# Kernel tuning notes

Measured on AMD Instinct MI355X. Metric: run time of the kernel, lower is better.

The kernel has to match this reference:

```python
import jax, jax.numpy as jnp
import numpy as np

K = 3  # kernel_size

def _extract_patches(x):
    # x: (b, n, h, w) -> (b, n, K*K, h, w), stride=1, padding=1 (zeros), row-major kernel order like nn.Unfold
    b, n, h, w = x.shape
    xp = jnp.pad(x, ((0, 0), (0, 0), (1, 1), (1, 1)))
    slices = [xp[:, :, i:i + h, j:j + w] for i in range(K) for j in range(K)]
    return jnp.stack(slices, axis=2)

def _conv3x3(x, w, b):
    # x: (b, cin, h, w), w: (cout, cin, 3, 3)
    y = jax.lax.conv_general_dilated(
        x, w, window_strides=(1, 1), padding=((1, 1), (1, 1)),
        dimension_numbers=('NCHW', 'OIHW', 'NCHW'))
    return y + b[None, :, None, None]

def setup_inputs() -> dict:
    key = jax.random.key(0)
    ks = jax.random.split(key, 6)
    b, n, h, w = 8, 256, 64, 64
    cout, r = 256, 4
    cm = n // r
    s = lambda fan: 1.0 / np.sqrt(fan)
    return {
        'x':    jax.random.normal(ks[0], (b, n, h, w), jnp.float32),
        'w_c1': jax.random.normal(ks[1], (cm, n), jnp.float32) * s(n),
        'b_c1': jnp.zeros((cm,), jnp.float32),
        'w_c2': jax.random.normal(ks[2], (n, cm), jnp.float32) * s(cm),
        'b_c2': jnp.zeros((n,), jnp.float32),
        'w_d1': jax.random.normal(ks[3], (cm, n, 3, 3), jnp.float32) * s(n * 9),
        'b_d1': jnp.zeros((cm,), jnp.float32),
        'w_d2': jax.random.normal(ks[4], (K * K, cm), jnp.float32) * s(cm),
        'b_d2': jnp.zeros((K * K,), jnp.float32),
        'W':    jax.random.normal(ks[5], (cout, n, K * K), jnp.float32) * s(n * K * K),
    }

def reference(x, w_c1, b_c1, w_c2, b_c2, w_d1, b_d1, w_d2, b_d2, W):
    # channel attention branch: 1x1 -> ReLU -> 1x1, output (b, n, h, w)
    yc = jax.nn.relu(jnp.einsum('bnhw,mn->bmhw', x, w_c1) + b_c1[None, :, None, None])
    c = jnp.einsum('bmhw,nm->bnhw', yc, w_c2) + b_c2[None, :, None, None]
    # kernel (spatial) attention branch: 3x3 -> ReLU -> 1x1, output (b, K*K, h, w)
    yd = jax.nn.relu(_conv3x3(x, w_d1, b_d1))
    d = jnp.einsum('bmhw,km->bkhw', yd, w_d2) + b_d2[None, :, None, None]
    # unfold and modulate: (b, n, K*K, h, w)
    patches = _extract_patches(x)
    attn = 1.0 + jnp.tanh(d[:, None, :, :, :] + c[:, :, None, :, :])
    # conv3d with (out, in, K*K, 1, 1) weight == per-pixel contraction over (n, K*K)
    out = jnp.einsum('bnkhw,onk->bohw', patches * attn, W)
    return out
```

## Files before the change

### kernel.cpp

```cpp
#include <hip/hip_runtime.h>
#include <hip/hip_bf16.h>
#include <stdint.h>

typedef __attribute__((ext_vector_type(8))) short bf16x8;
typedef __attribute__((ext_vector_type(4))) short bf16x4;
typedef __attribute__((ext_vector_type(4))) float f32x4;
typedef __attribute__((ext_vector_type(4))) int   i32x4;
typedef __attribute__((ext_vector_type(2))) int   i32x2;

#define DEV static __device__ __forceinline__

DEV float bf2f(short s) {
    unsigned u = ((unsigned)(unsigned short)s) << 16;
    return __builtin_bit_cast(float, u);
}
DEV short f2bf(float f) {
    unsigned u = __builtin_bit_cast(unsigned, f);
    unsigned r = u + 0x7fffu + ((u >> 16) & 1u);
    return (short)(r >> 16);
}
DEV unsigned cvt_pk_bf16(float lo, float hi) {
    unsigned r;
    asm("v_cvt_pk_bf16_f32 %0, %1, %2" : "=v"(r) : "v"(lo), "v"(hi));
    return r;
}

#define PTOT 32768
#define NEXP2 (-2.885390081777927f)

#define WS_WC1F 0
#define WS_WC2F 32768
#define WS_WD1F 65536
#define WS_WF   360448
#define WS_EKT  1540096
#define WS_EN   2719744
#define WS_XT   19496960

__global__ __launch_bounds__(256) void k_prep_all(const float* __restrict__ W, const float* __restrict__ w_d1,
                                              const float* __restrict__ w_c1, const float* __restrict__ w_c2,
                                              const float* __restrict__ x,
                                              short* __restrict__ Wf, short* __restrict__ wd1f,
                                              short* __restrict__ wc1f, short* __restrict__ wc2f,
                                              short* __restrict__ xT8) {
    __shared__ short t[64 * 74];
    const int tid = threadIdx.x;
    if (blockIdx.x < 3008) {
        int tt = blockIdx.x * 256 + tid;
        if (tt < 589824) {
            int i = tt & 7, lane = (tt >> 3) & 63, ot = (tt >> 9) & 15, kt = tt >> 13;
            int o = ot * 16 + (lane & 15);
            int n = (kt & 7) * 32 + (lane >> 4) * 8 + i;
            Wf[tt] = f2bf(2.0f * W[o * 2304 + n * 9 + (kt >> 3)]);
        } else if (tt < 589824 + 147456) {
            int t2 = tt - 589824;
            int i = t2 & 7, lane = (t2 >> 3) & 63, wv = (t2 >> 9) & 3, kc = t2 >> 11;
            int m = wv * 16 + (lane & 15);
            int n = (kc & 7) * 32 + (lane >> 4) * 8 + i;
            wd1f[t2] = f2bf(w_d1[m * 2304 + n * 9 + (kc >> 3)]);
        } else if (tt < 589824 + 147456 + 16384) {
            int t3 = tt - (589824 + 147456);
            int i = t3 & 7, lane = (t3 >> 3) & 63, wv = (t3 >> 9) & 3, s = t3 >> 11;
            int m = wv * 16 + (lane & 15);
            int n = s * 32 + (lane >> 4) * 8 + i;
            wc1f[t3] = f2bf(w_c1[m * 256 + n]);
        } else if (tt < 589824 + 147456 + 32768) {
            int t4 = tt - (589824 + 147456 + 16384);
            int i = t4 & 7, lane = (t4 >> 3) & 63, ot = (t4 >> 9) & 15, s = t4 >> 13;
            int o = ot * 16 + (lane & 15);
            int kk = s * 32 + (lane >> 4) * 8 + i;
            wc2f[t4] = f2bf(w_c2[o * 64 + kk]);
        }
        return;
    }
    const int bid = blockIdx.x - 3008;
    const int rw = ((bid & 7) << 6) + (bid >> 3);
    const int b = rw >> 6, hr = rw & 63;
    const int hp = hr + 1;
    #define XI(HP, NP, WP) ((((size_t)(b) * 66 + (HP)) * 32 + (NP)) * 66 + (WP)) * 8
    if (tid < 64) {
        int np = tid & 31, wp = (tid & 32) ? 65 : 0;
        *(i32x4*)(xT8 + XI(hp, np, wp)) = i32x4{0, 0, 0, 0};
    }
    if (hr == 0) {
        for (int i = tid; i < 2 * 32 * 66; i += 256) {
            int pl = (i >= 32 * 66) ? 65 : 0;
            int rem = (i >= 32 * 66) ? i - 32 * 66 : i;
            int np = rem / 66, wp = rem - np * 66;
            *(i32x4*)(xT8 + XI(pl, np, wp)) = i32x4{0, 0, 0, 0};
        }
    }
    const int dn = tid >> 6, w = tid & 63;
    for (int p = 0; p < 4; ++p) {
        __syncthreads();
        #pragma unroll
        for (int jj = 0; jj < 16; ++jj) {
            int n = p * 64 + dn * 16 + jj;
            t[w * 74 + dn * 16 + jj] = f2bf(x[(((size_t)(b * 256 + n) * 64) + hr) * 64 + w]);
        }
        __syncthreads();
        #pragma unroll
        for (int q = 0; q < 2; ++q) {
            int nl = q * 4 + dn;
            *(bf16x8*)(xT8 + XI(hp, p * 8 + nl, w + 1)) = *(const bf16x8*)(t + w * 74 + nl * 8);
        }
    }
    #undef XI
}

#define BR_YD_OFF  9216
#define BR_ENT_OFF (BR_YD_OFF + 17152)
#define BR_TOTAL   (BR_ENT_OFF + 33792)

__global__ __launch_bounds__(512, 4) void k_branch(const short* __restrict__ xT8,
        const float* __restrict__ b_c1, const float* __restrict__ b_c2,
        const float* __restrict__ b_d1, const float* __restrict__ w_d2, const float* __restrict__ b_d2,
        const short* __restrict__ wc1f, const short* __restrict__ wc2f, const short* __restrict__ wd1f,
        short* __restrict__ enF, float* __restrict__ ekT) {
    extern __shared__ char smem[];
    short* yc  = (short*)smem;
    float* ydl = (float*)(smem + BR_YD_OFF);
    short* ent = (short*)(smem + BR_ENT_OFF);

    const int rw = ((blockIdx.x & 7) << 6) + (blockIdx.x >> 3);
    const int b = rw >> 6, h = rw & 63;
    const int p0 = rw << 6;
    const int tid = threadIdx.x;
    const int lane = tid & 63, wave = tid >> 6;
    const int l16 = lane & 15, lg = lane >> 4;
    const int wn = wave & 3, wm = wave >> 2;
    const int cm = wn * 16 + l16;
    const size_t b66h = (size_t)(b * 66 + h);
    const int wcol = wm * 32 + l16;

    #define CONV_A(DST, KC) {                                                           \
        int k9_ = (KC) >> 3;                                                            \
        int kh_ = (k9_ * 11) >> 5, kw_ = k9_ - 3 * kh_;                                 \
        const short* xa_ = xT8 + (((b66h + kh_) * 32 + ((KC) & 7) * 4 + lg) * 66        \
                                  + wcol + kw_) * 8;                                    \
        DST[0] = *(const bf16x8*)(xa_);                                                 \
        DST[1] = *(const bf16x8*)(xa_ + 128);                                           \
    }

    {
        f32x4 acc[2] = {};
        const short* wp_ = wc1f + wn * 512 + lane * 8;
        const short* xg1 = xT8 + (((b66h + 1) * 32 + lg) * 66 + wcol + 1) * 8;
        bf16x8 bcur = *(const bf16x8*)(wp_);
        bf16x8 a0 = *(const bf16x8*)(xg1), a1 = *(const bf16x8*)(xg1 + 128);
        #pragma unroll
        for (int s = 0; s < 8; ++s) {
            bf16x8 bc = bcur, c0 = a0, c1 = a1;
            if (s < 7) {
                bcur = *(const bf16x8*)(wp_ + (s + 1) * 2048);
                a0 = *(const bf16x8*)(xg1 + (s + 1) * 2112);
                a1 = *(const bf16x8*)(xg1 + (s + 1) * 2112 + 128);
            }
            acc[0] = __builtin_amdgcn_mfma_f32_16x16x32_bf16(c0, bc, acc[0], 0, 0, 0);
            acc[1] = __builtin_amdgcn_mfma_f32_16x16x32_bf16(c1, bc, acc[1], 0, 0, 0);
        }
        float bias = b_c1[cm];
        #pragma unroll
        for (int mt = 0; mt < 2; ++mt)
            #pragma unroll
            for (int r = 0; r < 4; ++r) {
                int px = wm * 32 + mt * 16 + lg * 4 + r;
                float v = acc[mt][r] + bias;
                yc[px * 72 + cm] = f2bf(v > 0.f ? v : 0.f);
            }
    }

    {
        f32x4 acc[2] = {};
        const short* wp_ = wd1f + wn * 512 + lane * 8;
        bf16x8 b0 = *(const bf16x8*)(wp_);
        bf16x8 b1 = *(const bf16x8*)(wp_ + 2048);
        bf16x8 b2 = *(const bf16x8*)(wp_ + 4096);
        bf16x8 aA[2], aB[2], aC[2];
        CONV_A(aA, 0) CONV_A(aB, 1) CONV_A(aC, 2)
        for (int kc = 0; kc < 72; kc += 3) {
            {
                bf16x8 c0 = aA[0], c1 = aA[1], bc = b0;
                int cn = (kc + 3 < 72) ? kc + 3 : 71;
                CONV_A(aA, cn)
                b0 = *(const bf16x8*)(wp_ + cn * 2048);
                acc[0] = __builtin_amdgcn_mfma_f32_16x16x32_bf16(c0, bc, acc[0], 0, 0, 0);
                acc[1] = __builtin_amdgcn_mfma_f32_16x16x32_bf16(c1, bc, acc[1], 0, 0, 0);
            }
            {
                bf16x8 c0 = aB[0], c1 = aB[1], bc = b1;
                int cn = (kc + 4 < 72) ? kc + 4 : 71;
                CONV_A(aB, cn)
                b1 = *(const bf16x8*)(wp_ + cn * 2048);
                acc[0] = __builtin_amdgcn_mfma_f32_16x16x32_bf16(c0, bc, acc[0], 0, 0, 0);
                acc[1] = __builtin_amdgcn_mfma_f32_16x16x32_bf16(c1, bc, acc[1], 0, 0, 0);
            }
            {
                bf16x8 c0 = aC[0], c1 = aC[1], bc = b2;
                int cn = (kc + 5 < 72) ? kc + 5 : 71;
                CONV_A(aC, cn)
                b2 = *(const bf16x8*)(wp_ + cn * 2048);
                acc[0] = __builtin_amdgcn_mfma_f32_16x16x32_bf16(c0, bc, acc[0], 0, 0, 0);
                acc[1] = __builtin_amdgcn_mfma_f32_16x16x32_bf16(c1, bc, acc[1], 0, 0, 0);
            }
        }
        float bias = b_d1[cm];
        #pragma unroll
        for (int mt = 0; mt < 2; ++mt)
            #pragma unroll
            for (int r = 0; r < 4; ++r) {
                int px = wm * 32 + mt * 16 + lg * 4 + r;
                float v = acc[mt][r] + bias;
                ydl[px * 67 + cm] = v > 0.f ? v : 0.f;
            }
    }
    #undef CONV_A
    __syncthreads();

    {
        f32x4 acc[2][4] = {};
        #pragma unroll
        for (int s = 0; s < 2; ++s) {
            int k0 = s * 32;
            bf16x8 afr[2], bfr[4];
            #pragma unroll
            for (int mt = 0; mt < 2; ++mt)
                afr[mt] = *(const bf16x8*)(yc + (wm * 32 + mt * 16 + l16) * 72 + k0 + lg * 8);
            #pragma unroll
            for (int nt = 0; nt < 4; ++nt)
                bfr[nt] = *(const bf16x8*)(wc2f + s * 8192 + (wn * 4 + nt) * 512 + lane * 8);
            #pragma unroll
            for (int mt = 0; mt < 2; ++mt)
                #pragma unroll
                for (int nt = 0; nt < 4; ++nt)
                    acc[mt][nt] = __builtin_amdgcn_mfma_f32_16x16x32_bf16(afr[mt], bfr[nt], acc[mt][nt], 0, 0, 0);
        }
        #pragma unroll
        for (int nt = 0; nt < 4; ++nt) {
            int nc = wn * 64 + nt * 16 + l16;
            float bias = b_c2[nc];
            #pragma unroll
            for (int mt = 0; mt < 2; ++mt)
                #pragma unroll
                for (int r = 0; r < 4; ++r) {
                    int px = wm * 32 + mt * 16 + lg * 4 + r;
                    float cv = acc[mt][nt][r] + bias;
                    ent[px * 264 + nc] = f2bf(exp2f(NEXP2 * cv));
                }
        }
    }

    for (int t = tid; t < 576; t += 512) {
        int k = t >> 6, px = t & 63;
        float sum = b_d2[k];
        const float* yr = ydl + px * 67;
        const float* wr = w_d2 + k * 64;
        #pragma unroll 8
        for (int m = 0; m < 64; ++m) sum += yr[m] * wr[m];
        ekT[(size_t)k * PTOT + p0 + px] = exp2f(NEXP2 * sum);
    }
    __syncthreads();

    for (int i = tid; i < 2048; i += 512) {
        int px = i & 63, seg = i >> 6;
        *(bf16x8*)(enF + (size_t)p0 * 256 + (seg >> 2) * 2048 + (seg & 3) * 512 + px * 8)
            = *(const bf16x8*)(ent + px * 264 + seg * 8);
    }
}

#define FN5_Z1    4096
#define FN5_EKL   8192
#define FN5_TOTAL 10496

__global__ __launch_bounds__(512, 4) void k_final(const short* __restrict__ xT8,
        const short* __restrict__ Wf, const short* __restrict__ enF, const float* __restrict__ ekT,
        float* __restrict__ out) {
    extern __shared__ char smem[];
    short* z0  = (short*)smem;
    short* z1  = (short*)(smem + FN5_Z1);
    float* ekl = (float*)(smem + FN5_EKL);

    const int rw = ((blockIdx.x & 7) << 6) + (blockIdx.x >> 3);
    const int b = rw >> 6, h = rw & 63;
    const int p0 = rw << 6;
    const int tid = threadIdx.x;
    const int lane = tid & 63, wave = tid >> 6;
    const int l16 = lane & 15, lg = lane >> 4;

    for (int i = tid; i < 576; i += 512)
        ekl[i] = ekT[(size_t)(i >> 6) * PTOT + p0 + (i & 63)];

    const size_t b66h = (size_t)(b * 66 + h);
    const int zpx = lane;
    const int wh = wave >> 1, wl = wave & 1;
    const short* xb0 = xT8 + (b66h * 32 + wh) * 528 + zpx * 8 + wl * 4;
    bf16x4 e_regs[8];
    {
        const short* enb = enF + (size_t)p0 * 256 + wh * 512 + zpx * 8 + wl * 4;
        #pragma unroll
        for (int c8 = 0; c8 < 8; ++c8) e_regs[c8] = *(const bf16x4*)(enb + c8 * 2048);
    }
    const int zwoff = (zpx >> 4) * 512 + ((zpx & 15) + wh * 16) * 8 + wl * 4;
    const short* wb0 = Wf + (wave * 2 + 0) * 512 + lane * 8;
    const short* wb1 = Wf + (wave * 2 + 1) * 512 + lane * 8;

    bf16x4 xr;
    #define XLOAD(KC2) {                                                                \
        int k3_ = (KC2) >> 3, c8_ = (KC2) & 7;                                          \
        int kh_ = (k3_ * 11) >> 5, kw_ = k3_ - 3 * kh_;                                 \
        xr = *(const bf16x4*)(xb0 + kh_ * 16896 + c8_ * 2112 + kw_ * 8);                \
    }
    #define ZBUILD(ZBUF, EKROW, EIDX) {                                                 \
        bf16x4 er = e_regs[EIDX];                                                       \
        float ekv = ekl[(EKROW) * 64 + zpx];                                            \
        float q0 = __builtin_fmaf(ekv, bf2f(er[0]), 1.0f);                              \
        float q1 = __builtin_fmaf(ekv, bf2f(er[1]), 1.0f);                              \
        float q2 = __builtin_fmaf(ekv, bf2f(er[2]), 1.0f);                              \
        float q3 = __builtin_fmaf(ekv, bf2f(er[3]), 1.0f);                              \
        i32x2 zz;                                                                       \
        zz[0] = cvt_pk_bf16(bf2f(xr[0]) * __builtin_amdgcn_rcpf(q0),                    \
                            bf2f(xr[1]) * __builtin_amdgcn_rcpf(q1));                   \
        zz[1] = cvt_pk_bf16(bf2f(xr[2]) * __builtin_amdgcn_rcpf(q2),                    \
                            bf2f(xr[3]) * __builtin_amdgcn_rcpf(q3));                   \
        *(i32x2*)((ZBUF) + zwoff) = zz;                                                 \
    }

    bf16x8 Be[2], Bo[2];
    Be[0] = *(const bf16x8*)(wb0);          Be[1] = *(const bf16x8*)(wb1);
    Bo[0] = *(const bf16x8*)(wb0 + 8192);   Bo[1] = *(const bf16x8*)(wb1 + 8192);
    XLOAD(0)
    __syncthreads();
    ZBUILD(z0, 0, 0)
    XLOAD(1)
    __syncthreads();

    f32x4 acc[4][2] = {};

    #define STEP(C8, P1, P2, EKROW) {                                                   \
        short* zcur = ((C8) & 1) ? z1 : z0;                                             \
        short* znxt = ((C8) & 1) ? z0 : z1;                                             \
        bf16x8 bc0, bc1;                                                                \
        if ((C8) & 1) { bc0 = Bo[0]; bc1 = Bo[1]; } else { bc0 = Be[0]; bc1 = Be[1]; }  \
        if (P2) {    \
            int kb2_ = (k3 * 8 + (C8) + 2) * 8192;                                      \
            if ((C8) & 1) { Bo[0] = *(const bf16x8*)(wb0 + kb2_);                       \
                            Bo[1] = *(const bf16x8*)(wb1 + kb2_); }                     \
            else          { Be[0] = *(const bf16x8*)(wb0 + kb2_);                       \
                            Be[1] = *(const bf16x8*)(wb1 + kb2_); }                     \
        }                                                                               \
        if (P1) ZBUILD(znxt, EKROW, ((C8) + 1) & 7)                                     \
        if (P2) XLOAD(k3 * 8 + (C8) + 2)                                                \
        bf16x8 afr[4];                                                                  \
        _Pragma("unroll")                                                               \
        for (int mt = 0; mt < 4; ++mt)                                                  \
            afr[mt] = *(const bf16x8*)(zcur + mt * 512 + lane * 8);                     \
        __builtin_amdgcn_s_setprio(1);                                                  \
        _Pragma("unroll")                                                               \
        for (int mt = 0; mt < 4; ++mt) {                                                \
            acc[mt][0] = __builtin_amdgcn_mfma_f32_16x16x32_bf16(afr[mt], bc0, acc[mt][0], 0, 0, 0); \
            acc[mt][1] = __builtin_amdgcn_mfma_f32_16x16x32_bf16(afr[mt], bc1, acc[mt][1], 0, 0, 0); \
        }                                                                               \
        __builtin_amdgcn_s_setprio(0);                                                  \
        __syncthreads();                                                                \
    }

    for (int k3 = 0; k3 < 8; ++k3) {
        STEP(0, 1, 1, k3) STEP(1, 1, 1, k3) STEP(2, 1, 1, k3) STEP(3, 1, 1, k3)
        STEP(4, 1, 1, k3) STEP(5, 1, 1, k3) STEP(6, 1, 1, k3) STEP(7, 1, 1, k3 + 1)
    }
    {
        const int k3 = 8;
        STEP(0, 1, 1, k3) STEP(1, 1, 1, k3) STEP(2, 1, 1, k3) STEP(3, 1, 1, k3)
        STEP(4, 1, 1, k3) STEP(5, 1, 1, k3) STEP(6, 1, 0, k3) STEP(7, 0, 0, k3)
    }
    #undef STEP
    #undef ZBUILD
    #undef XLOAD

    #pragma unroll
    for (int mt = 0; mt < 4; ++mt)
        #pragma unroll
        for (int nt = 0; nt < 2; ++nt) {
            int o = wave * 32 + nt * 16 + l16;
            float* d = out + (((size_t)b * 256 + o) * 64 + h) * 64 + mt * 16 + lg * 4;
            *(f32x4*)d = acc[mt][nt];
        }
}

extern "C" void kernel_launch(void* const* d_in, const int* in_sizes, int n_in,
                              void* d_out, int out_size, void* d_ws, size_t ws_size,
                              hipStream_t stream) {
    const float* x    = (const float*)d_in[0];
    const float* w_c1 = (const float*)d_in[1];
    const float* b_c1 = (const float*)d_in[2];
    const float* w_c2 = (const float*)d_in[3];
    const float* b_c2 = (const float*)d_in[4];
    const float* w_d1 = (const float*)d_in[5];
    const float* b_d1 = (const float*)d_in[6];
    const float* w_d2 = (const float*)d_in[7];
    const float* b_d2 = (const float*)d_in[8];
    const float* Wt   = (const float*)d_in[9];
    float* out = (float*)d_out;
    char* ws = (char*)d_ws;

    short* wc1f = (short*)(ws + WS_WC1F);
    short* wc2f = (short*)(ws + WS_WC2F);
    short* wd1f = (short*)(ws + WS_WD1F);
    short* Wf   = (short*)(ws + WS_WF);
    float* ekT  = (float*)(ws + WS_EKT);
    short* enF  = (short*)(ws + WS_EN);
    short* xT8  = (short*)(ws + WS_XT);

    (void)hipFuncSetAttribute((const void*)k_branch, hipFuncAttributeMaxDynamicSharedMemorySize, BR_TOTAL);
    (void)hipFuncSetAttribute((const void*)k_final,  hipFuncAttributeMaxDynamicSharedMemorySize, FN5_TOTAL);

    k_prep_all<<<3520, 256, 0, stream>>>(Wt, w_d1, w_c1, w_c2, x, Wf, wd1f, wc1f, wc2f, xT8);
    k_branch<<<512, 512, BR_TOTAL, stream>>>(xT8, b_c1, b_c2, b_d1, w_d2, b_d2, wc1f, wc2f, wd1f, enF, ekT);
    k_final<<<512, 512, FN5_TOTAL, stream>>>(xT8, Wf, enF, ekT, out);
}
```

Baseline: 106.8 us.

## Use four LDS z-buffers in k_final to halve barriers per K step

Replaces the double-buffered LDS staging of the modulated patch tile with a four-slot ring, so each barrier now covers two MFMA K-chunks instead of one. Two x registers (xrA/xrB) alternate so the z tiles for chunks +2 and +3 are built while the current pair is consumed. This removes half of the __syncthreads in the main loop and gives more room to overlap loads with MFMA work. In exchange it uses more LDS per block (about 18.7KB instead of about 10.5KB) and more registers, which could reduce occupancy.

```diff
diff --git a/kernel.cpp b/kernel.cpp
--- a/kernel.cpp
+++ b/kernel.cpp
@@ -267,17 +267,18 @@
     }
 }
 
-#define FN5_Z1    4096
-#define FN5_EKL   8192
-#define FN5_TOTAL 10496
+#define FN6_EKL   16384
+#define FN6_TOTAL 18688
 
 __global__ __launch_bounds__(512, 4) void k_final(const short* __restrict__ xT8,
         const short* __restrict__ Wf, const short* __restrict__ enF, const float* __restrict__ ekT,
         float* __restrict__ out) {
     extern __shared__ char smem[];
-    short* z0  = (short*)smem;
-    short* z1  = (short*)(smem + FN5_Z1);
-    float* ekl = (float*)(smem + FN5_EKL);
+    short* zq0 = (short*)smem;
+    short* zq1 = (short*)(smem + 4096);
+    short* zq2 = (short*)(smem + 8192);
+    short* zq3 = (short*)(smem + 12288);
+    float* ekl = (float*)(smem + FN6_EKL);
 
     const int rw = ((blockIdx.x & 7) << 6) + (blockIdx.x >> 3);
     const int b = rw >> 6, h = rw & 63;
@@ -303,13 +304,20 @@
     const short* wb0 = Wf + (wave * 2 + 0) * 512 + lane * 8;
     const short* wb1 = Wf + (wave * 2 + 1) * 512 + lane * 8;
 
-    bf16x4 xr;
-    #define XLOAD(KC2) {                                                                \
+    #define ZQ(I) ((I) == 0 ? zq0 : (I) == 1 ? zq1 : (I) == 2 ? zq2 : zq3)
+
+    bf16x4 xrA, xrB;
+    #define XLOADA(KC2) {                                                               \
         int k3_ = (KC2) >> 3, c8_ = (KC2) & 7;                                          \
         int kh_ = (k3_ * 11) >> 5, kw_ = k3_ - 3 * kh_;                                 \
-        xr = *(const bf16x4*)(xb0 + kh_ * 16896 + c8_ * 2112 + kw_ * 8);                \
-    }
-    #define ZBUILD(ZBUF, EKROW, EIDX) {                                                 \
+        xrA = *(const bf16x4*)(xb0 + kh_ * 16896 + c8_ * 2112 + kw_ * 8);               \
+    }
+    #define XLOADB(KC2) {                                                               \
+        int k3_ = (KC2) >> 3, c8_ = (KC2) & 7;                                          \
+        int kh_ = (k3_ * 11) >> 5, kw_ = k3_ - 3 * kh_;                                 \
+        xrB = *(const bf16x4*)(xb0 + kh_ * 16896 + c8_ * 2112 + kw_ * 8);               \
+    }
+    #define ZBUILDX(ZBUF, EKROW, EIDX, XR) {                                            \
         bf16x4 er = e_regs[EIDX];                                                       \
         float ekv = ekl[(EKROW) * 64 + zpx];                                            \
         float q0 = __builtin_fmaf(ekv, bf2f(er[0]), 1.0f);                              \
@@ -317,64 +325,80 @@
         float q2 = __builtin_fmaf(ekv, bf2f(er[2]), 1.0f);                              \
         float q3 = __builtin_fmaf(ekv, bf2f(er[3]), 1.0f);                              \
         i32x2 zz;                                                                       \
-        zz[0] = cvt_pk_bf16(bf2f(xr[0]) * __builtin_amdgcn_rcpf(q0),                    \
-                            bf2f(xr[1]) * __builtin_amdgcn_rcpf(q1));                   \
-        zz[1] = cvt_pk_bf16(bf2f(xr[2]) * __builtin_amdgcn_rcpf(q2),                    \
-                            bf2f(xr[3]) * __builtin_amdgcn_rcpf(q3));                   \
+        zz[0] = cvt_pk_bf16(bf2f(XR[0]) * __builtin_amdgcn_rcpf(q0),                    \
+                            bf2f(XR[1]) * __builtin_amdgcn_rcpf(q1));                   \
+        zz[1] = cvt_pk_bf16(bf2f(XR[2]) * __builtin_amdgcn_rcpf(q2),                    \
+                            bf2f(XR[3]) * __builtin_amdgcn_rcpf(q3));                   \
         *(i32x2*)((ZBUF) + zwoff) = zz;                                                 \
     }
 
     bf16x8 Be[2], Bo[2];
     Be[0] = *(const bf16x8*)(wb0);          Be[1] = *(const bf16x8*)(wb1);
     Bo[0] = *(const bf16x8*)(wb0 + 8192);   Bo[1] = *(const bf16x8*)(wb1 + 8192);
-    XLOAD(0)
+    XLOADA(0) XLOADB(1)
     __syncthreads();
-    ZBUILD(z0, 0, 0)
-    XLOAD(1)
+    ZBUILDX(zq0, 0, 0, xrA)
+    ZBUILDX(zq1, 0, 1, xrB)
+    XLOADA(2) XLOADB(3)
     __syncthreads();
 
     f32x4 acc[4][2] = {};
 
-    #define STEP(C8, P1, P2, EKROW) {                                                   \
-        short* zcur = ((C8) & 1) ? z1 : z0;                                             \
-        short* znxt = ((C8) & 1) ? z0 : z1;                                             \
-        bf16x8 bc0, bc1;                                                                \
-        if ((C8) & 1) { bc0 = Bo[0]; bc1 = Bo[1]; } else { bc0 = Be[0]; bc1 = Be[1]; }  \
-        if (P2) {    \
-            int kb2_ = (k3 * 8 + (C8) + 2) * 8192;                                      \
-            if ((C8) & 1) { Bo[0] = *(const bf16x8*)(wb0 + kb2_);                       \
-                            Bo[1] = *(const bf16x8*)(wb1 + kb2_); }                     \
-            else          { Be[0] = *(const bf16x8*)(wb0 + kb2_);                       \
-                            Be[1] = *(const bf16x8*)(wb1 + kb2_); }                     \
-        }                                                                               \
-        if (P1) ZBUILD(znxt, EKROW, ((C8) + 1) & 7)                                     \
-        if (P2) XLOAD(k3 * 8 + (C8) + 2)                                                \
+    #define PHASE(C8, P1, P2, EKR) {                                                    \
+        short* zE = ZQ((C8) & 3);                                                       \
+        short* zO = ZQ(((C8) + 1) & 3);                                                 \
         bf16x8 afr[4];                                                                  \
         _Pragma("unroll")                                                               \
         for (int mt = 0; mt < 4; ++mt)                                                  \
-            afr[mt] = *(const bf16x8*)(zcur + mt * 512 + lane * 8);                     \
+            afr[mt] = *(const bf16x8*)(zE + mt * 512 + lane * 8);                       \
         __builtin_amdgcn_s_setprio(1);                                                  \
         _Pragma("unroll")                                                               \
         for (int mt = 0; mt < 4; ++mt) {                                                \
-            acc[mt][0] = __builtin_amdgcn_mfma_f32_16x16x32_bf16(afr[mt], bc0, acc[mt][0], 0, 0, 0); \
-            acc[mt][1] = __builtin_amdgcn_mfma_f32_16x16x32_bf16(afr[mt], bc1, acc[mt][1], 0, 0, 0); \
+            acc[mt][0] = __builtin_amdgcn_mfma_f32_16x16x32_bf16(afr[mt], Be[0], acc[mt][0], 0, 0, 0); \
+            acc[mt][1] = __builtin_amdgcn_mfma_f32_16x16x32_bf16(afr[mt], Be[1], acc[mt][1], 0, 0, 0); \
         }                                                                               \
         __builtin_amdgcn_s_setprio(0);                                                  \
+        if (P1) {                                                                       \
+            int kb2_ = (k3 * 8 + (C8) + 2) * 8192;                                      \
+            Be[0] = *(const bf16x8*)(wb0 + kb2_);                                       \
+            Be[1] = *(const bf16x8*)(wb1 + kb2_);                                       \
+            ZBUILDX(ZQ(((C8) + 2) & 3), EKR, ((C8) + 2) & 7, xrA)                       \
+        }                                                                               \
+        if (P2) XLOADA(k3 * 8 + (C8) + 4)                                               \
+        _Pragma("unroll")                                                               \
+        for (int mt = 0; mt < 4; ++mt)                                                  \
+            afr[mt] = *(const bf16x8*)(zO + mt * 512 + lane * 8);                       \
+        __builtin_amdgcn_s_setprio(1);                                                  \
+        _Pragma("unroll")                                                               \
+        for (int mt = 0; mt < 4; ++mt) {                                                \
+            acc[mt][0] = __builtin_amdgcn_mfma_f32_16x16x32_bf16(afr[mt], Bo[0], acc[mt][0], 0, 0, 0); \
+            acc[mt][1] = __builtin_amdgcn_mfma_f32_16x16x32_bf16(afr[mt], Bo[1], acc[mt][1], 0, 0, 0); \
+        }                                                                               \
+        __builtin_amdgcn_s_setprio(0);                                                  \
+        if (P1) {                                                                       \
+            int kb3_ = (k3 * 8 + (C8) + 3) * 8192;                                      \
+            Bo[0] = *(const bf16x8*)(wb0 + kb3_);                                       \
+            Bo[1] = *(const bf16x8*)(wb1 + kb3_);                                       \
+            ZBUILDX(ZQ(((C8) + 3) & 3), EKR, ((C8) + 3) & 7, xrB)                       \
+        }                                                                               \
+        if (P2) XLOADB(k3 * 8 + (C8) + 5)                                               \
         __syncthreads();                                                                \
     }
 
     for (int k3 = 0; k3 < 8; ++k3) {
-        STEP(0, 1, 1, k3) STEP(1, 1, 1, k3) STEP(2, 1, 1, k3) STEP(3, 1, 1, k3)
-        STEP(4, 1, 1, k3) STEP(5, 1, 1, k3) STEP(6, 1, 1, k3) STEP(7, 1, 1, k3 + 1)
+        PHASE(0, 1, 1, k3) PHASE(2, 1, 1, k3)
+        PHASE(4, 1, 1, k3) PHASE(6, 1, 1, k3 + 1)
     }
     {
         const int k3 = 8;
-        STEP(0, 1, 1, k3) STEP(1, 1, 1, k3) STEP(2, 1, 1, k3) STEP(3, 1, 1, k3)
-        STEP(4, 1, 1, k3) STEP(5, 1, 1, k3) STEP(6, 1, 0, k3) STEP(7, 0, 0, k3)
-    }
-    #undef STEP
-    #undef ZBUILD
-    #undef XLOAD
+        PHASE(0, 1, 1, k3) PHASE(2, 1, 1, k3)
+        PHASE(4, 1, 0, k3) PHASE(6, 0, 0, k3)
+    }
+    #undef PHASE
+    #undef ZBUILDX
+    #undef XLOADA
+    #undef XLOADB
+    #undef ZQ
 
     #pragma unroll
     for (int mt = 0; mt < 4; ++mt)
@@ -411,9 +435,9 @@
     short* xT8  = (short*)(ws + WS_XT);
 
     (void)hipFuncSetAttribute((const void*)k_branch, hipFuncAttributeMaxDynamicSharedMemorySize, BR_TOTAL);
-    (void)hipFuncSetAttribute((const void*)k_final,  hipFuncAttributeMaxDynamicSharedMemorySize, FN5_TOTAL);
+    (void)hipFuncSetAttribute((const void*)k_final,  hipFuncAttributeMaxDynamicSharedMemorySize, FN6_TOTAL);
 
     k_prep_all<<<3520, 256, 0, stream>>>(Wt, w_d1, w_c1, w_c2, x, Wf, wd1f, wc1f, wc2f, xT8);
     k_branch<<<512, 512, BR_TOTAL, stream>>>(xT8, b_c1, b_c2, b_d1, w_d2, b_d2, wc1f, wc2f, wd1f, enF, ekT);
-    k_final<<<512, 512, FN5_TOTAL, stream>>>(xT8, Wf, enF, ekT, out);
-}
+    k_final<<<512, 512, FN6_TOTAL, stream>>>(xT8, Wf, enF, ekT, out);
+}
```

Result: faster. 103.8 us (-2.7%).
